# Performance work log

Measured on AMD Instinct MI355X. Metric: run time of the kernel, lower is better.

## Reference

```python
import jax, jax.numpy as jnp
import numpy as np

NUM_EXPERTS = 64
TOP_K = 2
NUM_TOKENS = 16384
DIM = 4096


def setup_inputs() -> dict:
    key = jax.random.key(0)
    k1, k2, k3 = jax.random.split(key, 3)
    x = jax.random.normal(k1, (NUM_TOKENS, DIM), dtype=jnp.float32)
    top_scores = jax.random.uniform(k2, (NUM_TOKENS, TOP_K), dtype=jnp.float32)
    selected_experts_indices = jax.random.randint(k3, (NUM_TOKENS, TOP_K), 0, NUM_EXPERTS, dtype=jnp.int64 if jax.config.jax_enable_x64 else jnp.int32)
    num_tokens_per_expert = jnp.zeros((NUM_EXPERTS,), dtype=jnp.int32)
    return {
        "x": x,
        "top_scores": top_scores,
        "selected_experts_indices": selected_experts_indices,
        "num_tokens_per_expert": num_tokens_per_expert,
    }


def reference(x, top_scores, selected_experts_indices, num_tokens_per_expert):
    # ---- dispatch ----
    flat_experts = selected_experts_indices.reshape(-1)          # (T*K,)
    # histc over expert ids (torch.histc returns float)
    counts = jnp.zeros((NUM_EXPERTS,), dtype=jnp.float32).at[flat_experts].add(1.0)
    # stable sort by expert id
    order = jnp.argsort(flat_experts, stable=True)               # (T*K,)
    top_scores_sorted = top_scores.reshape(-1)[order]            # (T*K,)
    token_idx = order // TOP_K                                   # (T*K,) original token per slot
    routed_input = x[token_idx]                                  # (T*K, D) gather
    # score_before_experts=True: scale in fp32, cast back
    routed_input = (routed_input.astype(jnp.float32) * top_scores_sorted[:, None]).astype(x.dtype)

    # ---- expert computation is identity here; routed_output = routed_input ----
    routed_output = routed_input

    # ---- combine: deterministic scatter-add back to original token order ----
    out = jnp.zeros((NUM_TOKENS, DIM), dtype=routed_output.dtype)
    out = out.at[token_idx].add(routed_output)
    return out, counts
```

## Files before the change

### kernel.cpp

```cpp
#include <hip/hip_runtime.h>

#define NUM_EXPERTS 64
#define TOP_K 2
#define NUM_TOKENS 16384
#define DIM 4096

__global__ __launch_bounds__(256) void moe_fused_kernel(
    const float* __restrict__ x,
    const float* __restrict__ scores,
    const int* __restrict__ experts,
    float* __restrict__ out,
    float* __restrict__ counts) {
    const int b = blockIdx.x;

    if (b < NUM_TOKENS) {
        const int t = b;
        const float s0 = scores[t * TOP_K + 0];
        const float s1 = scores[t * TOP_K + 1];
        const float s = s0 + s1;
        const float4* __restrict__ xin =
            reinterpret_cast<const float4*>(x + (size_t)t * DIM);
        float4* __restrict__ o = reinterpret_cast<float4*>(out + (size_t)t * DIM);
#pragma unroll
        for (int i = 0; i < 4; ++i) {
            const int idx = threadIdx.x + i * 256;
            float4 v = xin[idx];
            float4 r;
            r.x = v.x * s0 + v.x * s1;
            r.y = v.y * s0 + v.y * s1;
            r.z = v.z * s0 + v.z * s1;
            r.w = v.w * s0 + v.w * s1;
            o[idx] = r;
        }
        (void)s;
    } else {
        __shared__ int h[NUM_EXPERTS];
        if (threadIdx.x < NUM_EXPERTS) h[threadIdx.x] = 0;
        __syncthreads();
        const int4* __restrict__ e4 = reinterpret_cast<const int4*>(experts);
        const int n4 = (NUM_TOKENS * TOP_K) / 4;
        for (int i = threadIdx.x; i < n4; i += 256) {
            int4 v = e4[i];
            atomicAdd(&h[v.x], 1);
            atomicAdd(&h[v.y], 1);
            atomicAdd(&h[v.z], 1);
            atomicAdd(&h[v.w], 1);
        }
        __syncthreads();
        if (threadIdx.x < NUM_EXPERTS)
            counts[threadIdx.x] = (float)h[threadIdx.x];
    }
}

extern "C" void kernel_launch(void* const* d_in, const int* in_sizes, int n_in,
                              void* d_out, int out_size, void* d_ws, size_t ws_size,
                              hipStream_t stream) {
    const float* x = (const float*)d_in[0];
    const float* top_scores = (const float*)d_in[1];
    const int* experts = (const int*)d_in[2];

    float* out = (float*)d_out;
    float* counts = out + (size_t)NUM_TOKENS * DIM;

    moe_fused_kernel<<<NUM_TOKENS + 1, 256, 0, stream>>>(x, top_scores, experts,
                                                         out, counts);
}
```

Measured before the change: 107.1 us.

## Process eight rows per block, split histogram across blocks, use nontemporal access

The grid shrinks from one block per token to 2048 blocks that each stream eight rows, using nontemporal vector loads and stores. The single serial histogram block is replaced by 64 blocks that each count a slice of expert ids and merge their counts into global memory with float atomics. A memset launched before the kernel now zeroes the counts buffer. The aim is less launch and tail overhead, the serial histogram no longer sitting on the critical path, and less cache pollution. The cost is an extra memset launch plus global atomics.

```diff
diff --git a/kernel.cpp b/kernel.cpp
--- a/kernel.cpp
+++ b/kernel.cpp
@@ -4,6 +4,10 @@
 #define TOP_K 2
 #define NUM_TOKENS 16384
 #define DIM 4096
+#define NBLOCKS 2048
+#define ROWS_PER_BLOCK (NUM_TOKENS / NBLOCKS)
+
+typedef float f4 __attribute__((ext_vector_type(4)));
 
 __global__ __launch_bounds__(256) void moe_fused_kernel(
     const float* __restrict__ x,
@@ -13,33 +17,14 @@
     float* __restrict__ counts) {
     const int b = blockIdx.x;
 
-    if (b < NUM_TOKENS) {
-        const int t = b;
-        const float s0 = scores[t * TOP_K + 0];
-        const float s1 = scores[t * TOP_K + 1];
-        const float s = s0 + s1;
-        const float4* __restrict__ xin =
-            reinterpret_cast<const float4*>(x + (size_t)t * DIM);
-        float4* __restrict__ o = reinterpret_cast<float4*>(out + (size_t)t * DIM);
-#pragma unroll
-        for (int i = 0; i < 4; ++i) {
-            const int idx = threadIdx.x + i * 256;
-            float4 v = xin[idx];
-            float4 r;
-            r.x = v.x * s0 + v.x * s1;
-            r.y = v.y * s0 + v.y * s1;
-            r.z = v.z * s0 + v.z * s1;
-            r.w = v.w * s0 + v.w * s1;
-            o[idx] = r;
-        }
-        (void)s;
-    } else {
+    if (b < NUM_EXPERTS) {
         __shared__ int h[NUM_EXPERTS];
         if (threadIdx.x < NUM_EXPERTS) h[threadIdx.x] = 0;
         __syncthreads();
-        const int4* __restrict__ e4 = reinterpret_cast<const int4*>(experts);
-        const int n4 = (NUM_TOKENS * TOP_K) / 4;
-        for (int i = threadIdx.x; i < n4; i += 256) {
+        const int per_block = (NUM_TOKENS * TOP_K) / NUM_EXPERTS;
+        const int4* __restrict__ e4 =
+            reinterpret_cast<const int4*>(experts + b * per_block);
+        for (int i = threadIdx.x; i < per_block / 4; i += 256) {
             int4 v = e4[i];
             atomicAdd(&h[v.x], 1);
             atomicAdd(&h[v.y], 1);
@@ -47,8 +32,32 @@
             atomicAdd(&h[v.w], 1);
         }
         __syncthreads();
-        if (threadIdx.x < NUM_EXPERTS)
-            counts[threadIdx.x] = (float)h[threadIdx.x];
+        if (threadIdx.x < NUM_EXPERTS) {
+            int c = h[threadIdx.x];
+            if (c > 0) atomicAdd(&counts[threadIdx.x], (float)c);
+        }
+    }
+
+    const int row0 = b * ROWS_PER_BLOCK;
+#pragma unroll
+    for (int r = 0; r < ROWS_PER_BLOCK; ++r) {
+        const int t = row0 + r;
+        const float s0 = scores[t * TOP_K + 0];
+        const float s1 = scores[t * TOP_K + 1];
+        const f4* __restrict__ xin =
+            reinterpret_cast<const f4*>(x + (size_t)t * DIM);
+        f4* __restrict__ o = reinterpret_cast<f4*>(out + (size_t)t * DIM);
+#pragma unroll
+        for (int i = 0; i < 4; ++i) {
+            const int idx = threadIdx.x + i * 256;
+            f4 v = __builtin_nontemporal_load(&xin[idx]);
+            f4 rr;
+            rr[0] = v[0] * s0 + v[0] * s1;
+            rr[1] = v[1] * s0 + v[1] * s1;
+            rr[2] = v[2] * s0 + v[2] * s1;
+            rr[3] = v[3] * s0 + v[3] * s1;
+            __builtin_nontemporal_store(rr, &o[idx]);
+        }
     }
 }
 
@@ -62,6 +71,7 @@
     float* out = (float*)d_out;
     float* counts = out + (size_t)NUM_TOKENS * DIM;
 
-    moe_fused_kernel<<<NUM_TOKENS + 1, 256, 0, stream>>>(x, top_scores, experts,
-                                                         out, counts);
+    hipMemsetAsync(counts, 0, NUM_EXPERTS * sizeof(float), stream);
+    moe_fused_kernel<<<NBLOCKS, 256, 0, stream>>>(x, top_scores, experts, out,
+                                                  counts);
 }
```

Measured after the change: 102.9 us. -3.9%, faster.
